# Kernel optimization log

Measured on AMD Instinct MI355X. Metric: run time of the kernel, lower is better.

Reference implementation:

```python
import jax, jax.numpy as jnp
import numpy as np

B, S, D = 8, 1024, 2048
H, HD = 16, 128          # n_heads, head_dim (H*HD == D)
ROPE = 64                # rotary dims per head (front slice)
MAXB, MAXS = 10, 1024    # kv-cache buffer sizes (hardcoded in module)
START_POS = 0


def _apply_rope(x, cos_half, sin_half):
    # x: (BH, S, ROPE); cos/sin_half: (S, ROPE//2) -> tiled to (S, ROPE)
    cos_full = jnp.concatenate([cos_half, cos_half], axis=-1)
    sin_full = jnp.concatenate([sin_half, sin_half], axis=-1)
    half = x.shape[-1] // 2
    x1, x2 = x[..., :half], x[..., half:]
    rotated = jnp.concatenate([-x2, x1], axis=-1)
    return x * cos_full + rotated * sin_full


def setup_inputs() -> dict:
    key = jax.random.key(0)
    ks = jax.random.split(key, 6)
    sc = 0.02
    x = jax.random.normal(ks[0], (B, S, D), dtype=jnp.float32)
    wq = jax.random.normal(ks[1], (D, D), dtype=jnp.float32) * sc
    wk = jax.random.normal(ks[2], (D, D), dtype=jnp.float32) * sc
    wv = jax.random.normal(ks[3], (D, D), dtype=jnp.float32) * sc
    wo = jax.random.normal(ks[4], (D, D), dtype=jnp.float32) * sc
    bq = jnp.zeros((D,), jnp.float32)
    bk = jnp.zeros((D,), jnp.float32)
    bv = jnp.zeros((D,), jnp.float32)
    bo = jnp.zeros((D,), jnp.float32)
    # RoPE tables (HF "half" layout): angles over positions
    half = ROPE // 2
    inv_freq = 1.0 / (10000.0 ** (jnp.arange(half, dtype=jnp.float32) / half))
    ang = jnp.arange(S, dtype=jnp.float32)[:, None] * inv_freq[None, :]  # (S, half)
    cos_half = jnp.cos(ang)
    sin_half = jnp.sin(ang)
    mask = jnp.zeros((S, S), jnp.float32)  # additive mask, (seq, end_pos)
    cache_k = jnp.zeros((MAXB, MAXS, H * HD), jnp.float32)
    cache_v = jnp.zeros((MAXB, MAXS, H * HD), jnp.float32)
    return {
        "x": x, "wq": wq, "bq": bq, "wk": wk, "bk": bk, "wv": wv, "bv": bv,
        "wo": wo, "bo": bo, "cos_half": cos_half, "sin_half": sin_half,
        "mask": mask, "cache_k": cache_k, "cache_v": cache_v,
        "start_pos": START_POS,
    }


def reference(x, wq, bq, wk, bk, wv, bv, wo, bo, cos_half, sin_half, mask,
              cache_k, cache_v, start_pos):
    b, s, _ = x.shape
    end_pos = start_pos + s
    # QKV projections (torch Linear: y = x @ W.T + b)
    q = (x @ wq.T + bq).reshape(b, s, H, HD)
    k = (x @ wk.T + bk).reshape(b, s, H, HD)
    v = (x @ wv.T + bv).reshape(b, s, H, HD)
    # Partial RoPE on the first ROPE dims of each head
    q_head = q[..., :ROPE].transpose(0, 2, 1, 3).reshape(b * H, s, ROPE)
    k_head = k[..., :ROPE].transpose(0, 2, 1, 3).reshape(b * H, s, ROPE)
    q_head = _apply_rope(q_head, cos_half, sin_half)
    k_head = _apply_rope(k_head, cos_half, sin_half)
    q_head = q_head.reshape(b, H, s, ROPE).transpose(0, 2, 1, 3)
    k_head = k_head.reshape(b, H, s, ROPE).transpose(0, 2, 1, 3)
    q = jnp.concatenate([q_head, q[..., ROPE:]], axis=-1)
    k = jnp.concatenate([k_head, k[..., ROPE:]], axis=-1)
    # KV-cache write then read (start_pos is a static python int)
    cache_k = jax.lax.dynamic_update_slice(cache_k, k.reshape(b, s, H * HD), (0, start_pos, 0))
    cache_v = jax.lax.dynamic_update_slice(cache_v, v.reshape(b, s, H * HD), (0, start_pos, 0))
    k_cached = cache_k[:b, :end_pos].reshape(b, end_pos, H, HD)
    v_cached = cache_v[:b, :end_pos].reshape(b, end_pos, H, HD)
    # Unnormalized attention: no softmax, no scaling
    scores = jnp.einsum('bshd,bthd->bsht', q, k_cached)  # (B,S,H,T)
    scores = scores + mask[:, None, :]                   # (S,1,T) broadcast
    a_sum = jnp.einsum('bsht,bthd->bshd', scores, v_cached)
    out = a_sum.reshape(b, s, H * HD) @ wo.T + bo
    return out
```

## Files before the change

### kernel.cpp

```cpp
#include <hip/hip_runtime.h>
#include <stdint.h>

#define B_ 8
#define S_ 1024
#define D_ 2048
#define H_ 16
#define HD_ 128
#define NROW 8192
#define NQKV 6144

typedef __bf16 bf16;
typedef bf16  bf16x8 __attribute__((ext_vector_type(8)));
typedef bf16  bf16x4 __attribute__((ext_vector_type(4)));
typedef float f32x4  __attribute__((ext_vector_type(4)));

#define AS1 __attribute__((address_space(1)))
#define AS3 __attribute__((address_space(3)))

__device__ __forceinline__ void gl_lds16(const bf16* g, bf16* l) {
  __builtin_amdgcn_global_load_lds((AS1 void*)g, (AS3 void*)l, 16, 0, 0);
}

__global__ __launch_bounds__(256) void f2b4(const float* __restrict__ in,
                                            bf16* __restrict__ out, int n4) {
  int i = blockIdx.x * 256 + threadIdx.x;
  if (i >= n4) return;
  float4 v = reinterpret_cast<const float4*>(in)[i];
  bf16x4 o;
  o.x = (bf16)v.x; o.y = (bf16)v.y; o.z = (bf16)v.z; o.w = (bf16)v.w;
  reinterpret_cast<bf16x4*>(out)[i] = o;
}

__global__ void packb(const float* __restrict__ a, const float* __restrict__ b,
                      const float* __restrict__ c, float* __restrict__ o) {
  int i = blockIdx.x * 256 + threadIdx.x;
  if (i >= NQKV) return;
  o[i] = (i < 2048) ? a[i] : (i < 4096 ? b[i - 2048] : c[i - 4096]);
}

#define READ_A(QA, Ab)                                                        \
  _Pragma("unroll") for (int mi = 0; mi < 4; mi++)                            \
  _Pragma("unroll") for (int ks = 0; ks < 2; ks++)                            \
    af[mi][ks] = *reinterpret_cast<const bf16x8*>(                            \
        (Ab) + aoff + (((QA)*4 + mi)*2 + ks)*512);

#define READ_B(QB, Bb, BFR)                                                   \
  _Pragma("unroll") for (int ni = 0; ni < 2; ni++)                            \
  _Pragma("unroll") for (int ks = 0; ks < 2; ks++)                            \
    BFR[ni][ks] = *reinterpret_cast<const bf16x8*>(                           \
        (Bb) + boff + (((QB)*2 + ni)*2 + ks)*512);

#define MFMA_Q(QA, QB, BFR)                                                   \
  _Pragma("unroll") for (int mi = 0; mi < 4; mi++)                            \
  _Pragma("unroll") for (int ni = 0; ni < 2; ni++)                            \
  _Pragma("unroll") for (int ks = 0; ks < 2; ks++)                            \
    acc[(QA)*4 + mi][(QB)*2 + ni] = __builtin_amdgcn_mfma_f32_16x16x32_bf16(  \
        af[mi][ks], BFR[ni][ks], acc[(QA)*4 + mi][(QB)*2 + ni], 0, 0, 0);

#define STAGE_A(dst, koff)                                                    \
  gl_lds16(agA + (koff),                (dst) + wid*1024);                    \
  gl_lds16(agA + (koff) + 32,           (dst) + wid*1024 + 512);              \
  gl_lds16(agA + 128*la + (koff),       (dst) + (wid + 8)*1024);              \
  gl_lds16(agA + 128*la + (koff) + 32,  (dst) + (wid + 8)*1024 + 512);

#define STAGE_B(dst, koff)                                                    \
  gl_lds16(agB + (koff),                (dst) + wid*1024);                    \
  gl_lds16(agB + (koff) + 32,           (dst) + wid*1024 + 512);              \
  gl_lds16(agB + 128*lb + (koff),       (dst) + (wid + 8)*1024);              \
  gl_lds16(agB + 128*lb + (koff) + 32,  (dst) + (wid + 8)*1024 + 512);

template <typename CT, bool BIAS, bool ACCUM>
__global__ __launch_bounds__(512, 2) void gemm256(const bf16* __restrict__ A,
                                                  const bf16* __restrict__ Bm,
                                                  const float* __restrict__ bias,
                                                  CT* __restrict__ C,
                                                  int M, int N, int K,
                                                  long la, long lb, long lc,
                                                  long za, long zb, long zc) {
  extern __shared__ __align__(16) bf16 lds[];
  const int z = blockIdx.z;
  A  += (long)z * za;
  Bm += (long)z * zb;
  C  += (long)z * zc;
  const int tid  = threadIdx.x;
  const int wid  = tid >> 6;
  const int lane = tid & 63;
  const int wm0 = (wid >> 2) * 128;
  const int wn0 = (wid & 3) * 64;
  const int m0 = blockIdx.y * 256, n0 = blockIdx.x * 256;

  const int rr = lane >> 2;
  const int cc = ((lane & 3) * 8) ^ ((rr & 8) << 1);
  const bf16* agA = A  + (long)(m0 + wid * 16 + rr) * la + cc;
  const bf16* agB = Bm + (long)(n0 + wid * 16 + rr) * lb + cc;

  const int swz  = ((lane >> 4) * 8) ^ ((lane & 8) << 1);
  const int aoff = (wm0 >> 4) * 1024 + (lane & 15) * 32 + swz;
  const int boff = (wn0 >> 4) * 1024 + (lane & 15) * 32 + swz;

  f32x4 acc[8][4] = {};
  bf16x8 af[4][2], b0[2][2], b1[2][2];
  const int NT = K >> 6;

  { bf16* An = lds; bf16* Bn = lds + 16384;
    STAGE_A(An, 0); STAGE_B(Bn, 0); }
  asm volatile("s_waitcnt vmcnt(0)" ::: "memory");
  __builtin_amdgcn_s_barrier();

  for (int t = 0; t < NT; ++t) {
    const bf16* Ab = lds + (t & 1) * 32768;
    const bf16* Bb = Ab + 16384;
    bf16* An = lds + ((t & 1) ^ 1) * 32768;
    bf16* Bn = An + 16384;
    const long kn = (long)(t + 1) * 64;
    const bool pf = (t + 1) < NT;

    READ_A(0, Ab); READ_B(0, Bb, b0);
    if (pf) { STAGE_A(An, kn); }
    __builtin_amdgcn_s_barrier();
    asm volatile("s_waitcnt lgkmcnt(0)" ::: "memory");
    __builtin_amdgcn_sched_barrier(0);
    __builtin_amdgcn_s_setprio(1); MFMA_Q(0, 0, b0); __builtin_amdgcn_s_setprio(0);
    __builtin_amdgcn_s_barrier();

    READ_B(1, Bb, b1);
    if (pf) { STAGE_B(Bn, kn); }
    __builtin_amdgcn_s_barrier();
    asm volatile("s_waitcnt lgkmcnt(0)" ::: "memory");
    __builtin_amdgcn_sched_barrier(0);
    __builtin_amdgcn_s_setprio(1); MFMA_Q(0, 1, b1); __builtin_amdgcn_s_setprio(0);
    __builtin_amdgcn_s_barrier();

    READ_A(1, Ab);
    __builtin_amdgcn_s_barrier();
    asm volatile("s_waitcnt lgkmcnt(0)" ::: "memory");
    __builtin_amdgcn_sched_barrier(0);
    __builtin_amdgcn_s_setprio(1); MFMA_Q(1, 0, b0); __builtin_amdgcn_s_setprio(0);
    __builtin_amdgcn_s_barrier();

    __builtin_amdgcn_s_setprio(1); MFMA_Q(1, 1, b1); __builtin_amdgcn_s_setprio(0);
    asm volatile("s_waitcnt vmcnt(0)" ::: "memory");
    __builtin_amdgcn_s_barrier();
  }

#pragma unroll
  for (int mi = 0; mi < 8; mi++) {
#pragma unroll
    for (int ni = 0; ni < 4; ni++) {
      const int col = n0 + wn0 + ni * 16 + (lane & 15);
      float bv = 0.0f;
      if constexpr (BIAS) bv = bias[col];
      const long base = (long)(m0 + wm0 + mi * 16 + (lane >> 4) * 4) * lc + col;
#pragma unroll
      for (int r = 0; r < 4; r++) {
        float v = acc[mi][ni][r] + bv;
        if constexpr (ACCUM) v += (float)C[base + (long)r * lc];
        C[base + (long)r * lc] = (CT)v;
      }
    }
  }
}

template <typename CT, bool BIAS, bool ACCUM>
__global__ __launch_bounds__(256) void gemm_bt(const bf16* __restrict__ A,
                                               const bf16* __restrict__ Bm,
                                               const float* __restrict__ bias,
                                               CT* __restrict__ C,
                                               int M, int N, int K,
                                               long la, long lb, long lc,
                                               long za, long zb, long zc) {
  __shared__ __align__(16) bf16 As[128 * 32];
  __shared__ __align__(16) bf16 Bs[128 * 32];
  const int z = blockIdx.z;
  A  += (long)z * za;
  Bm += (long)z * zb;
  C  += (long)z * zc;
  const int tid = threadIdx.x;
  const int w = tid >> 6, l = tid & 63;
  const int wm = (w & 1) * 64, wn = (w >> 1) * 64;
  const int m0 = blockIdx.y * 128, n0 = blockIdx.x * 128;
  const int lr = l & 15, lk = (l >> 4) * 8;
  const int er = (l >> 4) * 4;

  const bf16* ag = A  + (long)(m0 + (tid >> 2)) * la + (tid & 3) * 8;
  const bf16* bg = Bm + (long)(n0 + (tid >> 2)) * lb + (tid & 3) * 8;
  bf16* al = As + (w * 16) * 32;
  bf16* bl = Bs + (w * 16) * 32;

  f32x4 acc[4][4] = {};

  for (int k0 = 0; k0 < K; k0 += 32) {
    gl_lds16(ag + k0,            al);
    gl_lds16(ag + 64 * la + k0,  al + 64 * 32);
    gl_lds16(bg + k0,            bl);
    gl_lds16(bg + 64 * lb + k0,  bl + 64 * 32);
    __syncthreads();
    bf16x8 afr[4], bfr[4];
#pragma unroll
    for (int mi = 0; mi < 4; mi++)
      afr[mi] = *reinterpret_cast<const bf16x8*>(As + (wm + mi * 16 + lr) * 32 + lk);
#pragma unroll
    for (int ni = 0; ni < 4; ni++)
      bfr[ni] = *reinterpret_cast<const bf16x8*>(Bs + (wn + ni * 16 + lr) * 32 + lk);
#pragma unroll
    for (int mi = 0; mi < 4; mi++)
#pragma unroll
      for (int ni = 0; ni < 4; ni++)
        acc[mi][ni] = __builtin_amdgcn_mfma_f32_16x16x32_bf16(afr[mi], bfr[ni], acc[mi][ni], 0, 0, 0);
    __syncthreads();
  }

#pragma unroll
  for (int mi = 0; mi < 4; mi++) {
#pragma unroll
    for (int ni = 0; ni < 4; ni++) {
      const int col = n0 + wn + ni * 16 + lr;
      float bv = 0.0f;
      if constexpr (BIAS) bv = bias[col];
      const long base = (long)(m0 + wm + mi * 16 + er) * lc + col;
#pragma unroll
      for (int r = 0; r < 4; r++) {
        float v = acc[mi][ni][r] + bv;
        if constexpr (ACCUM) v += (float)C[base + (long)r * lc];
        C[base + (long)r * lc] = (CT)v;
      }
    }
  }
}

__global__ __launch_bounds__(256) void rope_qk(bf16* __restrict__ QKV,
                                               const float* __restrict__ ch,
                                               const float* __restrict__ sh) {
  int idx = blockIdx.x * 256 + threadIdx.x;
  if (idx >= NROW * H_ * 2 * 32) return;
  int hd = idx & 31;
  int qk = (idx >> 5) & 1;
  int h  = (idx >> 6) & 15;
  int row = idx >> 10;
  int s = row & (S_ - 1);
  long base = (long)row * NQKV + qk * 2048 + h * HD_ + hd;
  float a  = (float)QKV[base];
  float b2 = (float)QKV[base + 32];
  float c = ch[s * 32 + hd], sn = sh[s * 32 + hd];
  QKV[base]      = (bf16)(a * c - b2 * sn);
  QKV[base + 32] = (bf16)(b2 * c + a * sn);
}

__global__ __launch_bounds__(256) void kvtrans(const bf16* __restrict__ QKV,
                                               bf16* __restrict__ Kt,
                                               bf16* __restrict__ Vt) {
  __shared__ unsigned short T[128 * 130];
  const int bid = blockIdx.x;
  const int tb = bid & 7, bh = (bid >> 3) & 127, kv = bid >> 10;
  const int b = bh >> 4, h = bh & 15;
  const int tid = threadIdx.x;
  const bf16* src = QKV + (long)(b * S_ + tb * 128) * NQKV + 2048 + kv * 2048 + h * HD_;
#pragma unroll
  for (int it = 0; it < 8; it++) {
    int chunk = it * 256 + tid;
    int r = chunk >> 4, hc = (chunk & 15) * 8;
    bf16x8 v = *reinterpret_cast<const bf16x8*>(src + (long)r * NQKV + hc);
    union { bf16x8 v8; unsigned short u[8]; } u8; u8.v8 = v;
#pragma unroll
    for (int j = 0; j < 8; j++) T[r * 130 + hc + j] = u8.u[j];
  }
  __syncthreads();
  bf16* dst = (kv ? Vt : Kt) + (long)bh * HD_ * S_ + tb * 128;
#pragma unroll
  for (int it = 0; it < 8; it++) {
    int chunk = it * 256 + tid;
    int hd = chunk >> 4, tc = (chunk & 15) * 8;
    union { bf16x8 v8; unsigned short u[8]; } u8;
#pragma unroll
    for (int j = 0; j < 8; j++) u8.u[j] = T[(tc + j) * 130 + hd];
    *reinterpret_cast<bf16x8*>(dst + (long)hd * S_ + tc) = u8.v8;
  }
}

__global__ __launch_bounds__(256) void qw2_gemm(const bf16* __restrict__ QKV,
                                                const bf16* __restrict__ W2,
                                                bf16* __restrict__ Ob) {
  __shared__ __align__(16) bf16 As[128 * 32];
  __shared__ __align__(16) bf16 Bs[128 * 32];
  const int z = blockIdx.z;
  const int b = z >> 4, h = z & 15;
  const int m0 = blockIdx.y * 128;
  const int tid = threadIdx.x;
  const int w = tid >> 6, l = tid & 63;
  const int wm = (w & 1) * 64, wn = (w >> 1) * 64;
  const int lr = l & 15, lk = (l >> 4) * 8;
  const int er = (l >> 4) * 4;

  const bf16* ag = QKV + (long)(b * S_ + m0 + (tid >> 2)) * NQKV + h * HD_ + (tid & 3) * 8;
  const bf16* bg = W2 + (long)z * (HD_ * HD_) + (tid >> 2) * HD_ + (tid & 3) * 8;
  bf16* al = As + (w * 16) * 32;
  bf16* bl = Bs + (w * 16) * 32;

  f32x4 acc[4][4] = {};

#pragma unroll
  for (int k0 = 0; k0 < HD_; k0 += 32) {
    gl_lds16(ag + k0,                   al);
    gl_lds16(ag + (long)64 * NQKV + k0, al + 64 * 32);
    gl_lds16(bg + k0,                   bl);
    gl_lds16(bg + 64 * HD_ + k0,        bl + 64 * 32);
    __syncthreads();
    bf16x8 afr[4], bfr[4];
#pragma unroll
    for (int mi = 0; mi < 4; mi++)
      afr[mi] = *reinterpret_cast<const bf16x8*>(As + (wm + mi * 16 + lr) * 32 + lk);
#pragma unroll
    for (int ni = 0; ni < 4; ni++)
      bfr[ni] = *reinterpret_cast<const bf16x8*>(Bs + (wn + ni * 16 + lr) * 32 + lk);
#pragma unroll
    for (int mi = 0; mi < 4; mi++)
#pragma unroll
      for (int ni = 0; ni < 4; ni++)
        acc[mi][ni] = __builtin_amdgcn_mfma_f32_16x16x32_bf16(afr[mi], bfr[ni], acc[mi][ni], 0, 0, 0);
    __syncthreads();
  }

#pragma unroll
  for (int mi = 0; mi < 4; mi++) {
#pragma unroll
    for (int ni = 0; ni < 4; ni++) {
      const int col = h * HD_ + wn + ni * 16 + lr;
#pragma unroll
      for (int r = 0; r < 4; r++) {
        const int sl = m0 + wm + mi * 16 + er + r;
        const long idx = (long)(b * S_ + sl) * D_ + col;
        Ob[idx] = (bf16)((float)Ob[idx] + acc[mi][ni][r]);
      }
    }
  }
}

extern "C" void kernel_launch(void* const* d_in, const int* in_sizes, int n_in,
                              void* d_out, int out_size, void* d_ws, size_t ws_size,
                              hipStream_t stream) {
  const float* x   = (const float*)d_in[0];
  const float* wq  = (const float*)d_in[1];
  const float* bq  = (const float*)d_in[2];
  const float* wk  = (const float*)d_in[3];
  const float* bk  = (const float*)d_in[4];
  const float* wv  = (const float*)d_in[5];
  const float* bv  = (const float*)d_in[6];
  const float* wo  = (const float*)d_in[7];
  const float* bo  = (const float*)d_in[8];
  const float* ch  = (const float*)d_in[9];
  const float* sh  = (const float*)d_in[10];
  const float* mask = (const float*)d_in[11];
  float* out = (float*)d_out;

  hipFuncSetAttribute(reinterpret_cast<const void*>(&gemm256<bf16, true, false>),
                      hipFuncAttributeMaxDynamicSharedMemorySize, 131072);
  hipFuncSetAttribute(reinterpret_cast<const void*>(&gemm256<bf16, false, false>),
                      hipFuncAttributeMaxDynamicSharedMemorySize, 131072);
  hipFuncSetAttribute(reinterpret_cast<const void*>(&gemm256<float, true, false>),
                      hipFuncAttributeMaxDynamicSharedMemorySize, 131072);

  char* ws = (char*)d_ws;
  bf16*  QKV   = (bf16*)(ws);
  bf16*  Vt    = (bf16*)(ws + 100663296);
  bf16*  Kt    = (bf16*)(ws + 134217728);
  bf16*  wob   = (bf16*)(ws + 167772160);
  float* bqkv  = (float*)(ws + 176160768);
  bf16*  maskb = (bf16*)(ws + 176185344);
  bf16*  W2    = (bf16*)(ws + 178282496);
  bf16*  Ob    = (bf16*)(ws + 182476800);
  bf16*  xb    = (bf16*)(ws + 216031232);
  bf16*  wqkvb = (bf16*)(ws + 249585664);

  f2b4<<<16384, 256, 0, stream>>>(x, xb, 4194304);
  f2b4<<<4096, 256, 0, stream>>>(wq, wqkvb,           1048576);
  f2b4<<<4096, 256, 0, stream>>>(wk, wqkvb + 4194304, 1048576);
  f2b4<<<4096, 256, 0, stream>>>(wv, wqkvb + 8388608, 1048576);
  f2b4<<<4096, 256, 0, stream>>>(wo, wob, 1048576);
  f2b4<<<1024, 256, 0, stream>>>(mask, maskb, 262144);
  packb<<<24, 256, 0, stream>>>(bq, bk, bv, bqkv);

  gemm256<bf16, true, false><<<dim3(24, 32, 1), 512, 131072, stream>>>(
      xb, wqkvb, bqkv, QKV, NROW, NQKV, D_,
      (long)D_, (long)D_, (long)NQKV, 0L, 0L, 0L);

  rope_qk<<<32768, 256, 0, stream>>>(QKV, ch, sh);
  kvtrans<<<2048, 256, 0, stream>>>(QKV, Kt, Vt);

  gemm_bt<bf16, false, false><<<dim3(1, 1, 128), 256, 0, stream>>>(
      Vt, Kt, nullptr, W2, HD_, HD_, S_,
      (long)S_, (long)S_, (long)HD_,
      (long)(HD_ * S_), (long)(HD_ * S_), (long)(HD_ * HD_));

  gemm256<bf16, false, false><<<dim3(8, 4, 8), 512, 131072, stream>>>(
      maskb, Vt, nullptr, Ob, S_, D_, S_,
      (long)S_, (long)S_, (long)D_,
      0L, (long)(D_ * S_), (long)(S_ * D_));

  qw2_gemm<<<dim3(1, 8, 128), 256, 0, stream>>>(QKV, W2, Ob);

  gemm256<float, true, false><<<dim3(8, 32, 1), 512, 131072, stream>>>(
      Ob, wob, bo, out, NROW, D_, D_,
      (long)D_, (long)D_, (long)D_, 0L, 0L, 0L);
}
```

Baseline: 642.8 us.

## Split GEMM K-tile into halves with partial vmcnt waits and fewer barriers

Reorganizes the bf16 GEMM main loop so each 64-wide K tile is processed as two 32-wide halves, with 16 MFMAs per step using four B fragments at once. Global-to-LDS staging is also split per half, and `s_waitcnt vmcnt(4)` waits only for the half about to be consumed, so the next half's loads stay in flight. Barriers per iteration drop from about seven to two. The aim is better overlap of memory traffic with MFMA work and less synchronization stall. The trade-off is more fragile ordering between LDS buffers and the waves that read them.

After: 632.9 us. Within noise of the previous version (-1.5%).

```diff
diff --git a/kernel.cpp b/kernel.cpp
--- a/kernel.cpp
+++ b/kernel.cpp
@@ -38,36 +38,33 @@
   o[i] = (i < 2048) ? a[i] : (i < 4096 ? b[i - 2048] : c[i - 4096]);
 }
 
-#define READ_A(QA, Ab)                                                        \
+#define READ_A4(QA, KS, Ab)                                                   \
   _Pragma("unroll") for (int mi = 0; mi < 4; mi++)                            \
-  _Pragma("unroll") for (int ks = 0; ks < 2; ks++)                            \
-    af[mi][ks] = *reinterpret_cast<const bf16x8*>(                            \
-        (Ab) + aoff + (((QA)*4 + mi)*2 + ks)*512);
-
-#define READ_B(QB, Bb, BFR)                                                   \
-  _Pragma("unroll") for (int ni = 0; ni < 2; ni++)                            \
-  _Pragma("unroll") for (int ks = 0; ks < 2; ks++)                            \
-    BFR[ni][ks] = *reinterpret_cast<const bf16x8*>(                           \
-        (Bb) + boff + (((QB)*2 + ni)*2 + ks)*512);
-
-#define MFMA_Q(QA, QB, BFR)                                                   \
+    af[mi] = *reinterpret_cast<const bf16x8*>(                                \
+        (Ab) + aoff + ((((QA)*4 + mi)*2) + (KS))*512);
+
+#define READ_B4(KS, Bb)                                                       \
+  _Pragma("unroll") for (int ni = 0; ni < 4; ni++)                            \
+    bfr[ni] = *reinterpret_cast<const bf16x8*>(                               \
+        (Bb) + boff + ((ni*2) + (KS))*512);
+
+#define MFMA16(QA)                                                            \
   _Pragma("unroll") for (int mi = 0; mi < 4; mi++)                            \
-  _Pragma("unroll") for (int ni = 0; ni < 2; ni++)                            \
-  _Pragma("unroll") for (int ks = 0; ks < 2; ks++)                            \
-    acc[(QA)*4 + mi][(QB)*2 + ni] = __builtin_amdgcn_mfma_f32_16x16x32_bf16(  \
-        af[mi][ks], BFR[ni][ks], acc[(QA)*4 + mi][(QB)*2 + ni], 0, 0, 0);
-
-#define STAGE_A(dst, koff)                                                    \
-  gl_lds16(agA + (koff),                (dst) + wid*1024);                    \
-  gl_lds16(agA + (koff) + 32,           (dst) + wid*1024 + 512);              \
-  gl_lds16(agA + 128*la + (koff),       (dst) + (wid + 8)*1024);              \
-  gl_lds16(agA + 128*la + (koff) + 32,  (dst) + (wid + 8)*1024 + 512);
-
-#define STAGE_B(dst, koff)                                                    \
-  gl_lds16(agB + (koff),                (dst) + wid*1024);                    \
-  gl_lds16(agB + (koff) + 32,           (dst) + wid*1024 + 512);              \
-  gl_lds16(agB + 128*lb + (koff),       (dst) + (wid + 8)*1024);              \
-  gl_lds16(agB + 128*lb + (koff) + 32,  (dst) + (wid + 8)*1024 + 512);
+  _Pragma("unroll") for (int ni = 0; ni < 4; ni++)                            \
+    acc[(QA)*4 + mi][ni] = __builtin_amdgcn_mfma_f32_16x16x32_bf16(           \
+        af[mi], bfr[ni], acc[(QA)*4 + mi][ni], 0, 0, 0);
+
+#define STAGE_H0(An, Bn, koff)                                                \
+  gl_lds16(agA + (koff),           (An) + wid*1024);                          \
+  gl_lds16(agA + 128*la + (koff),  (An) + (wid + 8)*1024);                    \
+  gl_lds16(agB + (koff),           (Bn) + wid*1024);                          \
+  gl_lds16(agB + 128*lb + (koff),  (Bn) + (wid + 8)*1024);
+
+#define STAGE_H1(An, Bn, koff)                                                \
+  gl_lds16(agA + (koff) + 32,          (An) + wid*1024 + 512);                \
+  gl_lds16(agA + 128*la + (koff) + 32, (An) + (wid + 8)*1024 + 512);          \
+  gl_lds16(agB + (koff) + 32,          (Bn) + wid*1024 + 512);                \
+  gl_lds16(agB + 128*lb + (koff) + 32, (Bn) + (wid + 8)*1024 + 512);
 
 template <typename CT, bool BIAS, bool ACCUM>
 __global__ __launch_bounds__(512, 2) void gemm256(const bf16* __restrict__ A,
@@ -99,13 +96,10 @@
   const int boff = (wn0 >> 4) * 1024 + (lane & 15) * 32 + swz;
 
   f32x4 acc[8][4] = {};
-  bf16x8 af[4][2], b0[2][2], b1[2][2];
   const int NT = K >> 6;
 
   { bf16* An = lds; bf16* Bn = lds + 16384;
-    STAGE_A(An, 0); STAGE_B(Bn, 0); }
-  asm volatile("s_waitcnt vmcnt(0)" ::: "memory");
-  __builtin_amdgcn_s_barrier();
+    STAGE_H0(An, Bn, 0); STAGE_H1(An, Bn, 0); }
 
   for (int t = 0; t < NT; ++t) {
     const bf16* Ab = lds + (t & 1) * 32768;
@@ -114,33 +108,34 @@
     bf16* Bn = An + 16384;
     const long kn = (long)(t + 1) * 64;
     const bool pf = (t + 1) < NT;
-
-    READ_A(0, Ab); READ_B(0, Bb, b0);
-    if (pf) { STAGE_A(An, kn); }
+    bf16x8 af[4], bfr[4];
+
+    asm volatile("s_waitcnt vmcnt(4)" ::: "memory");
     __builtin_amdgcn_s_barrier();
+    READ_A4(0, 0, Ab); READ_B4(0, Bb);
+    if (pf) { STAGE_H0(An, Bn, kn); }
     asm volatile("s_waitcnt lgkmcnt(0)" ::: "memory");
     __builtin_amdgcn_sched_barrier(0);
-    __builtin_amdgcn_s_setprio(1); MFMA_Q(0, 0, b0); __builtin_amdgcn_s_setprio(0);
-    __builtin_amdgcn_s_barrier();
-
-    READ_B(1, Bb, b1);
-    if (pf) { STAGE_B(Bn, kn); }
-    __builtin_amdgcn_s_barrier();
+    __builtin_amdgcn_s_setprio(1); MFMA16(0); __builtin_amdgcn_s_setprio(0);
+
+    READ_A4(1, 0, Ab);
     asm volatile("s_waitcnt lgkmcnt(0)" ::: "memory");
     __builtin_amdgcn_sched_barrier(0);
-    __builtin_amdgcn_s_setprio(1); MFMA_Q(0, 1, b1); __builtin_amdgcn_s_setprio(0);
+    __builtin_amdgcn_s_setprio(1); MFMA16(1); __builtin_amdgcn_s_setprio(0);
+
+    if (pf) asm volatile("s_waitcnt vmcnt(4)" ::: "memory");
+    else    asm volatile("s_waitcnt vmcnt(0)" ::: "memory");
     __builtin_amdgcn_s_barrier();
-
-    READ_A(1, Ab);
-    __builtin_amdgcn_s_barrier();
+    READ_A4(0, 1, Ab); READ_B4(1, Bb);
+    if (pf) { STAGE_H1(An, Bn, kn); }
     asm volatile("s_waitcnt lgkmcnt(0)" ::: "memory");
     __builtin_amdgcn_sched_barrier(0);
-    __builtin_amdgcn_s_setprio(1); MFMA_Q(1, 0, b0); __builtin_amdgcn_s_setprio(0);
-    __builtin_amdgcn_s_barrier();
-
-    __builtin_amdgcn_s_setprio(1); MFMA_Q(1, 1, b1); __builtin_amdgcn_s_setprio(0);
-    asm volatile("s_waitcnt vmcnt(0)" ::: "memory");
-    __builtin_amdgcn_s_barrier();
+    __builtin_amdgcn_s_setprio(1); MFMA16(0); __builtin_amdgcn_s_setprio(0);
+
+    READ_A4(1, 1, Ab);
+    asm volatile("s_waitcnt lgkmcnt(0)" ::: "memory");
+    __builtin_amdgcn_sched_barrier(0);
+    __builtin_amdgcn_s_setprio(1); MFMA16(1); __builtin_amdgcn_s_setprio(0);
   }
 
 #pragma unroll
```
